# Optimization experiments

Measured on AMD Instinct MI355X. Metric: run time of the kernel, lower is better.

The kernel has to match this reference:

```python
import jax, jax.numpy as jnp
import numpy as np

IN_F = 4096
OUT_F = 16384
TOKENS = 64


def setup_inputs() -> dict:
    key = jax.random.key(0)
    k1, k2, k3 = jax.random.split(key, 3)
    x = jax.random.normal(k1, (TOKENS, IN_F), dtype=jnp.float16)
    # int8-valued weights stored as int32 (same math after cast to fp16)
    weight = jax.random.randint(k2, (OUT_F, IN_F), -127, 127, dtype=jnp.int32)
    weight_scales = jax.random.uniform(k3, (OUT_F,), dtype=jnp.float16, minval=0.001, maxval=0.02)
    bias = jnp.zeros((1, OUT_F), dtype=jnp.float16)
    return {"x": x, "weight": weight, "weight_scales": weight_scales, "bias": bias}


def reference(x, weight, weight_scales, bias):
    # Dequantize int8 weight to fp16 with per-output-channel scale, then linear.
    w_fp16 = weight.astype(jnp.float16) * weight_scales[:, None]  # [out, in]
    y = jnp.dot(x, w_fp16.T) + bias  # [tokens, out]
    return y
```

## Files before the change

### kernel.cpp

```cpp
#include <hip/hip_runtime.h>
#include <hip/hip_bf16.h>
#include <hip/hip_fp16.h>

#define IN_F 4096
#define OUT_F 16384
#define TOKENS 64

#define NT 32
#define KT 128
#define KHALF 2048
#define NTILES 16
#define TILE_BYTES (NT * KT * 4)
#define BLOCK 256

typedef __attribute__((ext_vector_type(8))) short bf16x8;
typedef __attribute__((ext_vector_type(8))) unsigned short u16x8;
typedef __attribute__((ext_vector_type(4))) float f32x4;
typedef __attribute__((ext_vector_type(4))) int i32x4;

enum { F_BF16 = 0, F_FP16 = 1, F_FP32 = 2 };

__device__ __forceinline__ float dec_bf16(unsigned short h) {
    return __uint_as_float(((unsigned)h) << 16);
}
__device__ __forceinline__ float dec_fp16(unsigned short h) {
    __half_raw hr; hr.x = h;
    return __half2float(__half(hr));
}
__device__ __forceinline__ unsigned short enc_bf16_rne(float f) {
    unsigned u = __float_as_uint(f);
    u += 0x7FFFu + ((u >> 16) & 1u);
    return (unsigned short)(u >> 16);
}

__device__ __forceinline__ int detect_fmt16(const void* p, int lane, float lo, float hi) {
    unsigned short h = ((const unsigned short*)p)[lane];
    float vb = fabsf(dec_bf16(h));
    float vh = fabsf(dec_fp16(h));
    int cb = __popcll(__ballot(vb > lo && vb < hi));
    int ch = __popcll(__ballot(vh > lo && vh < hi));
    return (cb >= 56) ? F_BF16 : (ch >= 56) ? F_FP16 : F_FP32;
}
__device__ __forceinline__ int detect_wint(const int* w, int lane) {
    int v = w[lane];
    int ci = __popcll(__ballot(v >= -127 && v <= 127));
    return (ci >= 56) ? 1 : 0;
}

__global__ __launch_bounds__(256) void prep_x(const void* __restrict__ xv,
                                              unsigned short* __restrict__ xbf) {
    const int tid  = blockIdx.x * 256 + threadIdx.x;
    const int lane = threadIdx.x & 63;
    const int xf = detect_fmt16(xv, lane, 9.7e-4f, 64.0f);

    if (xf == F_BF16) {
        u16x8 a = ((const u16x8*)xv)[tid * 2];
        u16x8 b = ((const u16x8*)xv)[tid * 2 + 1];
        ((u16x8*)xbf)[tid * 2]     = a;
        ((u16x8*)xbf)[tid * 2 + 1] = b;
    } else if (xf == F_FP32) {
        u16x8 o[2];
        #pragma unroll
        for (int half = 0; half < 2; ++half) {
            f32x4 v0 = ((const f32x4*)xv)[tid * 4 + half * 2];
            f32x4 v1 = ((const f32x4*)xv)[tid * 4 + half * 2 + 1];
            #pragma unroll
            for (int j = 0; j < 4; ++j) {
                o[half][j]     = enc_bf16_rne(v0[j]);
                o[half][j + 4] = enc_bf16_rne(v1[j]);
            }
        }
        ((u16x8*)xbf)[tid * 2]     = o[0];
        ((u16x8*)xbf)[tid * 2 + 1] = o[1];
    } else {
        #pragma unroll
        for (int half = 0; half < 2; ++half) {
            u16x8 v = ((const u16x8*)xv)[tid * 2 + half];
            u16x8 o;
            #pragma unroll
            for (int j = 0; j < 8; ++j) o[j] = enc_bf16_rne(dec_fp16(v[j]));
            ((u16x8*)xbf)[tid * 2 + half] = o;
        }
    }
}

template <int WINT>
__device__ __forceinline__ void tile_compute(const char* __restrict__ buf,
                                             const unsigned short* __restrict__ xbf,
                                             int kbase, int ln, int kq, int row,
                                             f32x4 acc[4]) {
    const char*  bufb = buf + row * 512;
    const short* xs   = (const short*)xbf;
    #pragma unroll
    for (int kt = 0; kt < 4; ++kt) {
        const int c0 = kt * 8 + 2 * kq;
        i32x4 b0 = *(const i32x4*)(bufb + ((c0)     ^ ln) * 16);
        i32x4 b1 = *(const i32x4*)(bufb + ((c0 + 1) ^ ln) * 16);
        bf16x8 bfrag;
        #pragma unroll
        for (int j = 0; j < 4; ++j) {
            unsigned f0 = WINT ? __float_as_uint((float)b0[j]) : (unsigned)b0[j];
            unsigned f1 = WINT ? __float_as_uint((float)b1[j]) : (unsigned)b1[j];
            bfrag[j]     = (short)(f0 >> 16);
            bfrag[j + 4] = (short)(f1 >> 16);
        }
        const int kk = kbase + kt * 32 + kq * 8;
        bf16x8 a0 = *(const bf16x8*)(xs + (size_t)(ln     ) * IN_F + kk);
        bf16x8 a1 = *(const bf16x8*)(xs + (size_t)(ln + 16) * IN_F + kk);
        bf16x8 a2 = *(const bf16x8*)(xs + (size_t)(ln + 32) * IN_F + kk);
        bf16x8 a3 = *(const bf16x8*)(xs + (size_t)(ln + 48) * IN_F + kk);
        acc[0] = __builtin_amdgcn_mfma_f32_16x16x32_bf16(a0, bfrag, acc[0], 0, 0, 0);
        acc[1] = __builtin_amdgcn_mfma_f32_16x16x32_bf16(a1, bfrag, acc[1], 0, 0, 0);
        acc[2] = __builtin_amdgcn_mfma_f32_16x16x32_bf16(a2, bfrag, acc[2], 0, 0, 0);
        acc[3] = __builtin_amdgcn_mfma_f32_16x16x32_bf16(a3, bfrag, acc[3], 0, 0, 0);
    }
}

__global__ __launch_bounds__(BLOCK, 2) void w8a16_main(
    const void* __restrict__ xv_orig, const int* __restrict__ w,
    const void* __restrict__ sv, const void* __restrict__ bv,
    void* __restrict__ yv, const unsigned short* __restrict__ xbf) {

    __shared__ alignas(16) char lds[2][2][TILE_BYTES];

    const int tid  = threadIdx.x;
    const int wv   = tid >> 6;
    const int lane = tid & 63;
    const int ln   = lane & 15;
    const int kq   = lane >> 4;
    const int h    = wv >> 1;
    const int wl   = wv & 1;
    const int n0   = blockIdx.x * NT;

    const int xf = detect_fmt16(xv_orig, lane, 9.7e-4f, 64.0f);
    const int sf = detect_fmt16(sv, lane, 1.0e-4f, 0.25f);
    const int wi = detect_wint(w, lane);

    const int th   = tid >> 7;
    const int t127 = tid & 127;
    auto stage = [&](int tile, int dbuf) {
        #pragma unroll
        for (int j = 0; j < 8; ++j) {
            const int idx = j * 128 + t127;
            const int r   = idx >> 5;
            const int c   = idx & 31;
            const int cg  = c ^ (r & 15);
            const int* g = w + (size_t)(n0 + r) * IN_F + th * KHALF + tile * KT + cg * 4;
            char* l = &lds[th][dbuf][idx * 16];
            __builtin_amdgcn_global_load_lds(
                (const __attribute__((address_space(1))) unsigned int*)g,
                (__attribute__((address_space(3))) unsigned int*)l, 16, 0, 0);
        }
    };

    f32x4 acc[4] = {};
    const int row = 16 * wl + ln;

    stage(0, 0);
    __syncthreads();
    for (int t = 0; t < NTILES; ++t) {
        if (t + 1 < NTILES) stage(t + 1, (t + 1) & 1);
        const char* buf   = &lds[h][t & 1][0];
        const int   kbase = h * KHALF + t * KT;
        if (wi) tile_compute<1>(buf, xbf, kbase, ln, kq, row, acc);
        else    tile_compute<0>(buf, xbf, kbase, ln, kq, row, acc);
        __syncthreads();
    }

    float* red = (float*)&lds[0][0][0];
    if (h == 1) {
        #pragma unroll
        for (int i = 0; i < 4; ++i)
            #pragma unroll
            for (int r2 = 0; r2 < 4; ++r2)
                red[(wl * 64 + lane) * 16 + i * 4 + r2] = acc[i][r2];
    }
    __syncthreads();
    if (h == 0) {
        #pragma unroll
        for (int i = 0; i < 4; ++i)
            #pragma unroll
            for (int r2 = 0; r2 < 4; ++r2)
                acc[i][r2] += red[(wl * 64 + lane) * 16 + i * 4 + r2];

        const int n = n0 + row;
        float scale, bias;
        if (sf == F_FP32) {
            scale = ((const float*)sv)[n];
            bias  = ((const float*)bv)[n];
        } else if (sf == F_BF16) {
            scale = dec_bf16(((const unsigned short*)sv)[n]);
            bias  = dec_bf16(((const unsigned short*)bv)[n]);
        } else {
            scale = dec_fp16(((const unsigned short*)sv)[n]);
            bias  = dec_fp16(((const unsigned short*)bv)[n]);
        }

        #pragma unroll
        for (int i = 0; i < 4; ++i) {
            #pragma unroll
            for (int r2 = 0; r2 < 4; ++r2) {
                const int    m   = 16 * i + kq * 4 + r2;
                const float  val = acc[i][r2] * scale + bias;
                const size_t o   = (size_t)m * OUT_F + n;
                if (xf == F_FP32)      ((float*)yv)[o] = val;
                else if (xf == F_BF16) ((unsigned short*)yv)[o] = enc_bf16_rne(val);
                else                   ((__half*)yv)[o] = __float2half(val);
            }
        }
    }
}

extern "C" void kernel_launch(void* const* d_in, const int* in_sizes, int n_in,
                              void* d_out, int out_size, void* d_ws, size_t ws_size,
                              hipStream_t stream) {
    unsigned short* xbf = (unsigned short*)d_ws;
    prep_x<<<64, 256, 0, stream>>>(d_in[0], xbf);
    w8a16_main<<<OUT_F / NT, BLOCK, 0, stream>>>(d_in[0], (const int*)d_in[1],
                                                 d_in[2], d_in[3], d_out, xbf);
}
```

Measured before the change: 381.5 us.

## Load weight fragments directly from global memory instead of LDS double-buffer staging

Removes the LDS double-buffered staging of weight tiles via global_load_lds and the per-tile __syncthreads. Each lane now reads its 32-byte weight fragment straight from global memory into registers, with a 4x unrolled loop over 32-wide k-blocks. This drops block-level barriers and LDS traffic. In exchange, latency hiding relies on compiler scheduling and occupancy rather than explicit prefetch, and each lane's global reads are 32 bytes per row, strided across rows, which may coalesce less well.

Measured after the change: 415.1 us. 1.09x slower.

```diff
diff --git a/kernel.cpp b/kernel.cpp
--- a/kernel.cpp
+++ b/kernel.cpp
@@ -7,10 +7,8 @@
 #define TOKENS 64
 
 #define NT 32
-#define KT 128
 #define KHALF 2048
-#define NTILES 16
-#define TILE_BYTES (NT * KT * 4)
+#define NKB (KHALF / 32)
 #define BLOCK 256
 
 typedef __attribute__((ext_vector_type(8))) short bf16x8;
@@ -85,35 +83,27 @@
 }
 
 template <int WINT>
-__device__ __forceinline__ void tile_compute(const char* __restrict__ buf,
-                                             const unsigned short* __restrict__ xbf,
-                                             int kbase, int ln, int kq, int row,
-                                             f32x4 acc[4]) {
-    const char*  bufb = buf + row * 512;
-    const short* xs   = (const short*)xbf;
+__device__ __forceinline__ void kblock_compute(const int* __restrict__ wrow,
+                                               const short* __restrict__ xrow,
+                                               int kb, f32x4 acc[4]) {
+    i32x4 b0 = *(const i32x4*)(wrow + kb * 32);
+    i32x4 b1 = *(const i32x4*)(wrow + kb * 32 + 4);
+    bf16x8 a0 = *(const bf16x8*)(xrow + kb * 32);
+    bf16x8 a1 = *(const bf16x8*)(xrow + kb * 32 + 16 * IN_F);
+    bf16x8 a2 = *(const bf16x8*)(xrow + kb * 32 + 32 * IN_F);
+    bf16x8 a3 = *(const bf16x8*)(xrow + kb * 32 + 48 * IN_F);
+    bf16x8 bfrag;
     #pragma unroll
-    for (int kt = 0; kt < 4; ++kt) {
-        const int c0 = kt * 8 + 2 * kq;
-        i32x4 b0 = *(const i32x4*)(bufb + ((c0)     ^ ln) * 16);
-        i32x4 b1 = *(const i32x4*)(bufb + ((c0 + 1) ^ ln) * 16);
-        bf16x8 bfrag;
-        #pragma unroll
-        for (int j = 0; j < 4; ++j) {
-            unsigned f0 = WINT ? __float_as_uint((float)b0[j]) : (unsigned)b0[j];
-            unsigned f1 = WINT ? __float_as_uint((float)b1[j]) : (unsigned)b1[j];
-            bfrag[j]     = (short)(f0 >> 16);
-            bfrag[j + 4] = (short)(f1 >> 16);
-        }
-        const int kk = kbase + kt * 32 + kq * 8;
-        bf16x8 a0 = *(const bf16x8*)(xs + (size_t)(ln     ) * IN_F + kk);
-        bf16x8 a1 = *(const bf16x8*)(xs + (size_t)(ln + 16) * IN_F + kk);
-        bf16x8 a2 = *(const bf16x8*)(xs + (size_t)(ln + 32) * IN_F + kk);
-        bf16x8 a3 = *(const bf16x8*)(xs + (size_t)(ln + 48) * IN_F + kk);
-        acc[0] = __builtin_amdgcn_mfma_f32_16x16x32_bf16(a0, bfrag, acc[0], 0, 0, 0);
-        acc[1] = __builtin_amdgcn_mfma_f32_16x16x32_bf16(a1, bfrag, acc[1], 0, 0, 0);
-        acc[2] = __builtin_amdgcn_mfma_f32_16x16x32_bf16(a2, bfrag, acc[2], 0, 0, 0);
-        acc[3] = __builtin_amdgcn_mfma_f32_16x16x32_bf16(a3, bfrag, acc[3], 0, 0, 0);
+    for (int j = 0; j < 4; ++j) {
+        unsigned f0 = WINT ? __float_as_uint((float)b0[j]) : (unsigned)b0[j];
+        unsigned f1 = WINT ? __float_as_uint((float)b1[j]) : (unsigned)b1[j];
+        bfrag[j]     = (short)(f0 >> 16);
+        bfrag[j + 4] = (short)(f1 >> 16);
     }
+    acc[0] = __builtin_amdgcn_mfma_f32_16x16x32_bf16(a0, bfrag, acc[0], 0, 0, 0);
+    acc[1] = __builtin_amdgcn_mfma_f32_16x16x32_bf16(a1, bfrag, acc[1], 0, 0, 0);
+    acc[2] = __builtin_amdgcn_mfma_f32_16x16x32_bf16(a2, bfrag, acc[2], 0, 0, 0);
+    acc[3] = __builtin_amdgcn_mfma_f32_16x16x32_bf16(a3, bfrag, acc[3], 0, 0, 0);
 }
 
 __global__ __launch_bounds__(BLOCK, 2) void w8a16_main(
@@ -121,7 +111,7 @@
     const void* __restrict__ sv, const void* __restrict__ bv,
     void* __restrict__ yv, const unsigned short* __restrict__ xbf) {
 
-    __shared__ alignas(16) char lds[2][2][TILE_BYTES];
+    __shared__ float red[2048];
 
     const int tid  = threadIdx.x;
     const int wv   = tid >> 6;
@@ -136,38 +126,19 @@
     const int sf = detect_fmt16(sv, lane, 1.0e-4f, 0.25f);
     const int wi = detect_wint(w, lane);
 
-    const int th   = tid >> 7;
-    const int t127 = tid & 127;
-    auto stage = [&](int tile, int dbuf) {
-        #pragma unroll
-        for (int j = 0; j < 8; ++j) {
-            const int idx = j * 128 + t127;
-            const int r   = idx >> 5;
-            const int c   = idx & 31;
-            const int cg  = c ^ (r & 15);
-            const int* g = w + (size_t)(n0 + r) * IN_F + th * KHALF + tile * KT + cg * 4;
-            char* l = &lds[th][dbuf][idx * 16];
-            __builtin_amdgcn_global_load_lds(
-                (const __attribute__((address_space(1))) unsigned int*)g,
-                (__attribute__((address_space(3))) unsigned int*)l, 16, 0, 0);
-        }
-    };
+    const int row = 16 * wl + ln;
+    const int*   wrow = w + (size_t)(n0 + row) * IN_F + h * KHALF + kq * 8;
+    const short* xrow = (const short*)xbf + (size_t)ln * IN_F + h * KHALF + kq * 8;
 
     f32x4 acc[4] = {};
-    const int row = 16 * wl + ln;
-
-    stage(0, 0);
-    __syncthreads();
-    for (int t = 0; t < NTILES; ++t) {
-        if (t + 1 < NTILES) stage(t + 1, (t + 1) & 1);
-        const char* buf   = &lds[h][t & 1][0];
-        const int   kbase = h * KHALF + t * KT;
-        if (wi) tile_compute<1>(buf, xbf, kbase, ln, kq, row, acc);
-        else    tile_compute<0>(buf, xbf, kbase, ln, kq, row, acc);
-        __syncthreads();
+    if (wi) {
+        #pragma unroll 4
+        for (int kb = 0; kb < NKB; ++kb) kblock_compute<1>(wrow, xrow, kb, acc);
+    } else {
+        #pragma unroll 4
+        for (int kb = 0; kb < NKB; ++kb) kblock_compute<0>(wrow, xrow, kb, acc);
     }
 
-    float* red = (float*)&lds[0][0][0];
     if (h == 1) {
         #pragma unroll
         for (int i = 0; i < 4; ++i)
```
